# Optimization experiments

Measured on AMD Instinct MI355X. Metric: run time of the kernel, lower is better.

The kernel has to match this reference:

```python
import jax, jax.numpy as jnp
import numpy as np

B, C, W, H, X, Y = 2, 32, 256, 256, 512, 512


def _rbf(x1, x2, ls):
    # x1: [B, N], x2: [B, M] -> [B, N, M]; identical math to norms+matmul pw_dists2 on 1-d coords
    d2 = (x1[:, :, None] - x2[:, None, :]) ** 2
    return jnp.exp(-0.5 * d2 / ls ** 2)


def setup_inputs() -> dict:
    key = jax.random.key(0)
    k0, k1, k2, k3, k4 = jax.random.split(key, 5)
    return {
        "x_in_lon": jax.random.uniform(k0, (B, W), jnp.float32),
        "x_in_lat": jax.random.uniform(k1, (B, H), jnp.float32),
        "wt": jax.random.normal(k2, (B, C, W, H), jnp.float32),
        "x_out_lon": jax.random.uniform(k3, (B, X), jnp.float32),
        "x_out_lat": jax.random.uniform(k4, (B, Y), jnp.float32),
        "init_ls": jnp.full((1,), 0.1, jnp.float32),
    }


def reference(x_in_lon, x_in_lat, wt, x_out_lon, x_out_lat, init_ls):
    # density channel: 1 where data present, 0 where NaN; zero-fill NaNs in data
    dens = jnp.where(jnp.isnan(wt[:, 0:1]), 0.0, 1.0)
    wt_full = jnp.concatenate([dens, jnp.nan_to_num(wt)], axis=1)  # [B, C+1, W, H]
    ls = init_ls[0]
    w_lon = _rbf(x_in_lon, x_out_lon, ls)  # [B, W, X]
    w_lat = _rbf(x_in_lat, x_out_lat, ls)  # [B, H, Y]
    # separable 'OnToOn' contraction: [B,C+1,W,H] x [B,W,X] x [B,H,Y] -> [B,C+1,X,Y]
    ee = jnp.einsum('bcwh,bwx,bhy->bcxy', wt_full, w_lon, w_lat)
    d = jnp.clip(ee[:, 0:1], 1e-6, 1e5)
    return jnp.concatenate([ee[:, 0:1], ee[:, 1:] / d], axis=1)
```

## Files before the change

### kernel.cpp

```cpp
#include <hip/hip_runtime.h>
#include <cstddef>

#define B_ 2
#define C_ 32
#define CP 33
#define W_ 256
#define H_ 256
#define X_ 512
#define Y_ 512

typedef __bf16 bf16x8 __attribute__((ext_vector_type(8)));
typedef __bf16 bf16x4 __attribute__((ext_vector_type(4)));
typedef float  f32x4  __attribute__((ext_vector_type(4)));

#define AS1 __attribute__((address_space(1)))
#define AS3 __attribute__((address_space(3)))

__device__ __forceinline__ void gload16_lds(const void* g, void* l) {
    __builtin_amdgcn_global_load_lds((const AS1 void*)g, (AS3 void*)l, 16, 0, 0);
}


__global__ __launch_bounds__(256) void prep_kernel(
    const float* __restrict__ xin_lon, const float* __restrict__ xin_lat,
    const float* __restrict__ xout_lon, const float* __restrict__ xout_lat,
    const float* __restrict__ init_ls, const float* __restrict__ wt,
    __bf16* __restrict__ wlonF, __bf16* __restrict__ wlatF,
    __bf16* __restrict__ wt33F)
{
    __shared__ __bf16 tile[64 * 130];

    const int t = threadIdx.x;
    const int bid = blockIdx.x;
    float ls = init_ls[0];
    float cc = -0.5f / (ls * ls);

    if (bid < 528) {
        const int p  = bid >> 3, tl = bid & 7;
        const int wq = tl >> 1, hq = tl & 1;
        const int b  = p / CP, ch = p - b * CP;
        const float* src = (ch == 0)
            ? wt + ((size_t)b * C_) * (W_ * H_)
            : wt + ((size_t)b * C_ + (ch - 1)) * (W_ * H_);
        const int rowt = t >> 5, hl = (t & 31) * 4;
#pragma unroll
        for (int i = 0; i < 8; ++i) {
            int rl = i * 8 + rowt;
            const float* sp = src + (size_t)(wq * 64 + rl) * H_ + hq * 128 + hl;
            float4 v = *(const float4*)sp;
            bf16x4 ov;
            if (ch == 0) {
                ov[0] = (__bf16)((v.x != v.x) ? 0.f : 1.f);
                ov[1] = (__bf16)((v.y != v.y) ? 0.f : 1.f);
                ov[2] = (__bf16)((v.z != v.z) ? 0.f : 1.f);
                ov[3] = (__bf16)((v.w != v.w) ? 0.f : 1.f);
            } else {
                ov[0] = (__bf16)((v.x != v.x) ? 0.f : v.x);
                ov[1] = (__bf16)((v.y != v.y) ? 0.f : v.y);
                ov[2] = (__bf16)((v.z != v.z) ? 0.f : v.z);
                ov[3] = (__bf16)((v.w != v.w) ? 0.f : v.w);
            }
            *(bf16x4*)&tile[rl * 130 + hl] = ov;
        }
        __syncthreads();
        const int lane = t & 63, wave = t >> 6;
        __bf16* pb = wt33F + (size_t)p * 65536 + (size_t)(wq >> 1) * 32768;
        const int rfg0 = (wq & 1) * 4, ktg0 = hq * 4;
#pragma unroll
        for (int it = 0; it < 4; ++it) {
            int ci   = it * 4 + wave;
            int kt_l = ci >> 2, rf_l = ci & 3;
            int wl = rf_l * 16 + (lane & 15);
            int hl2 = kt_l * 32 + (lane >> 4) * 8;
            bf16x8 v = *(const bf16x8*)&tile[wl * 130 + hl2];
            *(bf16x8*)&pb[(size_t)((ktg0 + kt_l) * 8 + rfg0 + rf_l) * 512
                          + lane * 8] = v;
        }
    } else {
        int j = (bid - 528) * 256 + t;
        if (j < 32768) {
            int lane = j & 63, nf = (j >> 6) & 3, kt = (j >> 8) & 7;
            int xt = (j >> 11) & 7, b = j >> 14;
            int x  = xt * 64 + nf * 16 + (lane & 15);
            int k0 = kt * 32 + (lane >> 4) * 8;
            float xo = xout_lon[b * X_ + x];
            bf16x8 v;
#pragma unroll
            for (int e = 0; e < 8; ++e) {
                float d = xin_lon[b * W_ + k0 + e] - xo;
                v[e] = (__bf16)__expf(cc * d * d);
            }
            *(bf16x8*)&wlonF[(size_t)j * 8] = v;
        } else {
            int c = j - 32768;
            int lane = c & 63, bfr = (c >> 6) & 3, kt = (c >> 8) & 7;
            int yt = (c >> 11) & 7, b = c >> 14;
            int y  = yt * 64 + bfr * 16 + (lane & 15);
            int h0 = kt * 32 + (lane >> 4) * 8;
            float yo = xout_lat[b * Y_ + y];
            bf16x8 v;
#pragma unroll
            for (int e = 0; e < 8; ++e) {
                float d = xin_lat[b * H_ + h0 + e] - yo;
                v[e] = (__bf16)__expf(cc * d * d);
            }
            *(bf16x8*)&wlatF[(size_t)c * 8] = v;
        }
    }
}

__global__ __launch_bounds__(256, 4) void gemm_u(
    const __bf16* __restrict__ wt33F, const __bf16* __restrict__ wlatF,
    __bf16* __restrict__ U_F)
{
    __shared__ union SM {
        struct { __bf16 A[2][4096]; __bf16 Bt[2][2048]; } t;
        __bf16 th[8704];
    } sm;

    const int t    = threadIdx.x;
    const int lane = t & 63;
    const int wave = t >> 6;
    const int wm   = wave >> 1, wn = wave & 1;
    const int lrow = lane & 15, lkg = lane >> 4;

    const int xcd = blockIdx.x & 7, k = blockIdx.x >> 3;
    const int m   = xcd * 132 + k;
    const int p   = m >> 4, tile = m & 15;
    const int mtile = tile >> 3, ntile = tile & 7;
    const int bb = (p >= CP) ? 1 : 0;
    const __bf16* Abase = wt33F + ((size_t)(p * 2 + mtile)) * 32768;
    const __bf16* Bbase = wlatF + ((size_t)(bb * 8 + ntile)) * 16384;

    auto stage = [&](int buf, int kt) {
#pragma unroll
        for (int j = 0; j < 2; ++j) {
            int rf = j * 4 + wave;
            gload16_lds((const void*)(Abase + (size_t)(kt * 8 + rf) * 512 + lane * 8),
                        (void*)&sm.t.A[buf][rf * 512]);
        }
        gload16_lds((const void*)(Bbase + (size_t)(kt * 4 + wave) * 512 + lane * 8),
                    (void*)&sm.t.Bt[buf][wave * 512]);
    };

    f32x4 acc[4][2] = {};
    stage(0, 0);
#pragma unroll
    for (int kt = 0; kt < 8; ++kt) {
        const int buf = kt & 1;
        if (kt < 7) {
            stage(buf ^ 1, kt + 1);
            asm volatile("s_waitcnt vmcnt(3)" ::: "memory");
        } else {
            asm volatile("s_waitcnt vmcnt(0)" ::: "memory");
        }
        __builtin_amdgcn_s_barrier();
        bf16x8 af[4], bf[2];
#pragma unroll
        for (int mt = 0; mt < 4; ++mt)
            af[mt] = *(const bf16x8*)&sm.t.A[buf][((wm * 4 + mt) * 64 + lane) * 8];
#pragma unroll
        for (int nt = 0; nt < 2; ++nt)
            bf[nt] = *(const bf16x8*)&sm.t.Bt[buf][((wn * 2 + nt) * 64 + lane) * 8];
#pragma unroll
        for (int mt = 0; mt < 4; ++mt)
#pragma unroll
            for (int nt = 0; nt < 2; ++nt)
                acc[mt][nt] = __builtin_amdgcn_mfma_f32_16x16x32_bf16(
                    af[mt], bf[nt], acc[mt][nt], 0, 0, 0);
        __builtin_amdgcn_sched_barrier(0);
        __builtin_amdgcn_s_barrier();
    }

#pragma unroll
    for (int mt = 0; mt < 4; ++mt)
#pragma unroll
        for (int nt = 0; nt < 2; ++nt) {
            int yloc = wn * 32 + nt * 16 + lrow;
            int wloc = wm * 64 + mt * 16 + lkg * 4;
            f32x4 c = acc[mt][nt];
            bf16x4 v4;
            v4[0] = (__bf16)c[0]; v4[1] = (__bf16)c[1];
            v4[2] = (__bf16)c[2]; v4[3] = (__bf16)c[3];
            *(bf16x4*)&sm.th[yloc * 136 + wloc] = v4;
        }
    __syncthreads();
    __bf16* up = U_F + (size_t)p * 131072 + (size_t)ntile * 16384
                 + (size_t)mtile * 4 * 2048;
#pragma unroll
    for (int it = 0; it < 4; ++it) {
        int c2 = it * 256 + t;
        int ktl = c2 >> 8, rq = (c2 >> 6) & 3, ln = c2 & 63;
        int yloc = rq * 16 + (ln & 15);
        int w8   = ktl * 4 + (ln >> 4);
        bf16x8 v = *(const bf16x8*)&sm.th[yloc * 136 + w8 * 8];
        *(bf16x8*)&up[(size_t)(ktl * 4 + rq) * 512 + ln * 8] = v;
    }
}

__global__ __launch_bounds__(256, 2) void stage2_fused(
    const __bf16* __restrict__ wlonF, const __bf16* __restrict__ U_F,
    float* __restrict__ out)
{
    __shared__ __bf16 Ast[2][12288];

    const int t = threadIdx.x, lane = t & 63, wave = t >> 6;
    const int lrow = lane & 15, lkg = lane >> 4;
    const int wm = wave >> 1, wn = wave & 1;

    const int bid  = blockIdx.x;
    const int xcd  = bid & 7, q = bid >> 3;
    const int combo = (q >> 6) * 8 + xcd;
    const int b    = combo >> 3, g = combo & 7;
    const int tile = q & 63;
    const int yt   = tile >> 3, xt = tile & 7;
    const int x0   = xt * 64, y0 = yt * 64;

    const __bf16* lonF  = wlonF + (size_t)(b * 8 + xt) * 16384;
    const __bf16* Ubase = U_F + (size_t)(b * CP) * 131072 + (size_t)yt * 16384;

    auto stage = [&](int slot, int kt) {
#pragma unroll
        for (int i = 0; i < 6; ++i) {
            const int jf = wave * 6 + i;
            const __bf16* src;
            if (jf < 20) {
                const int jj = jf >> 2;
                const int ch = (jj == 0) ? 0 : (g * 4 + jj);
                src = Ubase + (size_t)ch * 131072
                      + (size_t)(kt * 4 + (jf & 3)) * 512 + lane * 8;
            } else {
                src = lonF + (size_t)(kt * 4 + (jf - 20)) * 512 + lane * 8;
            }
            gload16_lds((const void*)src, (void*)&Ast[slot][jf * 512]);
        }
    };

    stage(0, 0);

    f32x4 acc[5][2][2] = {};
#pragma unroll
    for (int kt = 0; kt < 8; ++kt) {
        const int slot = kt & 1;
        if (kt < 7) {
            stage(slot ^ 1, kt + 1);
            asm volatile("s_waitcnt vmcnt(6)" ::: "memory");
        } else {
            asm volatile("s_waitcnt vmcnt(0)" ::: "memory");
        }
        __builtin_amdgcn_s_barrier();
        bf16x8 af[5][2], bfv[2];
#pragma unroll
        for (int j = 0; j < 5; ++j)
#pragma unroll
            for (int mt = 0; mt < 2; ++mt)
                af[j][mt] = *(const bf16x8*)
                    &Ast[slot][((j * 4 + wm * 2 + mt) * 64 + lane) * 8];
#pragma unroll
        for (int nt = 0; nt < 2; ++nt)
            bfv[nt] = *(const bf16x8*)
                &Ast[slot][((20 + wn * 2 + nt) * 64 + lane) * 8];
#pragma unroll
        for (int j = 0; j < 5; ++j)
#pragma unroll
            for (int mt = 0; mt < 2; ++mt)
#pragma unroll
                for (int nt = 0; nt < 2; ++nt)
                    acc[j][mt][nt] = __builtin_amdgcn_mfma_f32_16x16x32_bf16(
                        af[j][mt], bfv[nt], acc[j][mt][nt], 0, 0, 0);
        __builtin_amdgcn_sched_barrier(0);
        __builtin_amdgcn_s_barrier();
    }

    f32x4 rec[2][2];
#pragma unroll
    for (int mt = 0; mt < 2; ++mt)
#pragma unroll
        for (int nt = 0; nt < 2; ++nt) {
            f32x4 c = acc[0][mt][nt], q2;
#pragma unroll
            for (int rr = 0; rr < 4; ++rr)
                q2[rr] = 1.0f / fminf(fmaxf(c[rr], 1e-6f), 1e5f);
            rec[mt][nt] = q2;
        }
    if (g == 0) {
        float* outc = out + (size_t)(b * CP) * (X_ * Y_);
#pragma unroll
        for (int mt = 0; mt < 2; ++mt)
#pragma unroll
            for (int nt = 0; nt < 2; ++nt) {
                int xg = x0 + (wn * 2 + nt) * 16 + lrow;
                int yg = y0 + (wm * 2 + mt) * 16 + lkg * 4;
                *(f32x4*)&outc[(size_t)xg * Y_ + yg] = acc[0][mt][nt];
            }
    }
#pragma unroll
    for (int j = 1; j < 5; ++j) {
        float* outc = out + (size_t)(b * CP + g * 4 + j) * (size_t)(X_ * Y_);
#pragma unroll
        for (int mt = 0; mt < 2; ++mt)
#pragma unroll
            for (int nt = 0; nt < 2; ++nt) {
                int xg = x0 + (wn * 2 + nt) * 16 + lrow;
                int yg = y0 + (wm * 2 + mt) * 16 + lkg * 4;
                f32x4 v = acc[j][mt][nt] * rec[mt][nt];
                *(f32x4*)&outc[(size_t)xg * Y_ + yg] = v;
            }
    }
}

extern "C" void kernel_launch(void* const* d_in, const int* in_sizes, int n_in,
                              void* d_out, int out_size, void* d_ws, size_t ws_size,
                              hipStream_t stream)
{
    const float* xin_lon  = (const float*)d_in[0];
    const float* xin_lat  = (const float*)d_in[1];
    const float* wt       = (const float*)d_in[2];
    const float* xout_lon = (const float*)d_in[3];
    const float* xout_lat = (const float*)d_in[4];
    const float* init_ls  = (const float*)d_in[5];
    float* out = (float*)d_out;

    __bf16* wlonF = (__bf16*)d_ws;
    __bf16* wlatF = wlonF + (size_t)B_ * X_ * W_;
    __bf16* wt33F = wlatF + (size_t)B_ * Y_ * H_;
    __bf16* U_F   = wt33F + (size_t)B_ * CP * W_ * H_;

    prep_kernel<<<784, 256, 0, stream>>>(xin_lon, xin_lat, xout_lon, xout_lat,
                                         init_ls, wt, wlonF, wlatF, wt33F);
    gemm_u<<<1056, 256, 0, stream>>>(wt33F, wlatF, U_F);
    stage2_fused<<<1024, 256, 0, stream>>>(wlonF, U_F, out);
}
```

Baseline: 46.08 us.

## Load MFMA fragments directly from global memory, dropping LDS staging in stage2

```diff
diff --git a/kernel.cpp b/kernel.cpp
--- a/kernel.cpp
+++ b/kernel.cpp
@@ -202,8 +202,6 @@
     const __bf16* __restrict__ wlonF, const __bf16* __restrict__ U_F,
     float* __restrict__ out)
 {
-    __shared__ __bf16 Ast[2][12288];
-
     const int t = threadIdx.x, lane = t & 63, wave = t >> 6;
     const int lrow = lane & 15, lkg = lane >> 4;
     const int wm = wave >> 1, wn = wave & 1;
@@ -216,50 +214,26 @@
     const int yt   = tile >> 3, xt = tile & 7;
     const int x0   = xt * 64, y0 = yt * 64;
 
-    const __bf16* lonF  = wlonF + (size_t)(b * 8 + xt) * 16384;
-    const __bf16* Ubase = U_F + (size_t)(b * CP) * 131072 + (size_t)yt * 16384;
-
-    auto stage = [&](int slot, int kt) {
-#pragma unroll
-        for (int i = 0; i < 6; ++i) {
-            const int jf = wave * 6 + i;
-            const __bf16* src;
-            if (jf < 20) {
-                const int jj = jf >> 2;
-                const int ch = (jj == 0) ? 0 : (g * 4 + jj);
-                src = Ubase + (size_t)ch * 131072
-                      + (size_t)(kt * 4 + (jf & 3)) * 512 + lane * 8;
-            } else {
-                src = lonF + (size_t)(kt * 4 + (jf - 20)) * 512 + lane * 8;
-            }
-            gload16_lds((const void*)src, (void*)&Ast[slot][jf * 512]);
-        }
-    };
-
-    stage(0, 0);
+    const __bf16* lonp = wlonF + (size_t)(b * 8 + xt) * 16384
+                         + (size_t)(wn * 2) * 512 + lane * 8;
+    const __bf16* Au   = U_F + (size_t)(b * CP) * 131072 + (size_t)yt * 16384
+                         + (size_t)(wm * 2) * 512 + lane * 8;
 
     f32x4 acc[5][2][2] = {};
 #pragma unroll
     for (int kt = 0; kt < 8; ++kt) {
-        const int slot = kt & 1;
-        if (kt < 7) {
-            stage(slot ^ 1, kt + 1);
-            asm volatile("s_waitcnt vmcnt(6)" ::: "memory");
-        } else {
-            asm volatile("s_waitcnt vmcnt(0)" ::: "memory");
-        }
-        __builtin_amdgcn_s_barrier();
         bf16x8 af[5][2], bfv[2];
 #pragma unroll
-        for (int j = 0; j < 5; ++j)
+        for (int j = 0; j < 5; ++j) {
+            const int ch = (j == 0) ? 0 : (g * 4 + j);
 #pragma unroll
             for (int mt = 0; mt < 2; ++mt)
-                af[j][mt] = *(const bf16x8*)
-                    &Ast[slot][((j * 4 + wm * 2 + mt) * 64 + lane) * 8];
+                af[j][mt] = *(const bf16x8*)(Au + (size_t)ch * 131072
+                                             + (size_t)(kt * 4 + mt) * 512);
+        }
 #pragma unroll
         for (int nt = 0; nt < 2; ++nt)
-            bfv[nt] = *(const bf16x8*)
-                &Ast[slot][((20 + wn * 2 + nt) * 64 + lane) * 8];
+            bfv[nt] = *(const bf16x8*)(lonp + (size_t)(kt * 4 + nt) * 512);
 #pragma unroll
         for (int j = 0; j < 5; ++j)
 #pragma unroll
@@ -268,8 +242,6 @@
                 for (int nt = 0; nt < 2; ++nt)
                     acc[j][mt][nt] = __builtin_amdgcn_mfma_f32_16x16x32_bf16(
                         af[j][mt], bfv[nt], acc[j][mt][nt], 0, 0, 0);
-        __builtin_amdgcn_sched_barrier(0);
-        __builtin_amdgcn_s_barrier();
     }
 
     f32x4 rec[2][2];
```

Result: slower. 68.77 us (+49.2%).

## Process two channel groups per block, keeping lon tile resident in LDS

Applied to the files above, without the earlier changes.

```diff
diff --git a/kernel.cpp b/kernel.cpp
--- a/kernel.cpp
+++ b/kernel.cpp
@@ -202,110 +202,119 @@
     const __bf16* __restrict__ wlonF, const __bf16* __restrict__ U_F,
     float* __restrict__ out)
 {
-    __shared__ __bf16 Ast[2][12288];
+    __shared__ __bf16 Blon[16384];
+    __shared__ __bf16 Ast[2][10240];
 
     const int t = threadIdx.x, lane = t & 63, wave = t >> 6;
     const int lrow = lane & 15, lkg = lane >> 4;
     const int wm = wave >> 1, wn = wave & 1;
 
     const int bid  = blockIdx.x;
-    const int xcd  = bid & 7, q = bid >> 3;
-    const int combo = (q >> 6) * 8 + xcd;
-    const int b    = combo >> 3, g = combo & 7;
-    const int tile = q & 63;
-    const int yt   = tile >> 3, xt = tile & 7;
+    const int xcd  = bid & 7, r = bid >> 3;
+    const int b    = xcd >> 2, gpair = xcd & 3;
+    const int yt   = r >> 3, xt = r & 7;
     const int x0   = xt * 64, y0 = yt * 64;
+    const int g0   = gpair * 2;
 
     const __bf16* lonF  = wlonF + (size_t)(b * 8 + xt) * 16384;
     const __bf16* Ubase = U_F + (size_t)(b * CP) * 131072 + (size_t)yt * 16384;
 
-    auto stage = [&](int slot, int kt) {
-#pragma unroll
-        for (int i = 0; i < 6; ++i) {
-            const int jf = wave * 6 + i;
-            const __bf16* src;
-            if (jf < 20) {
-                const int jj = jf >> 2;
-                const int ch = (jj == 0) ? 0 : (g * 4 + jj);
-                src = Ubase + (size_t)ch * 131072
-                      + (size_t)(kt * 4 + (jf & 3)) * 512 + lane * 8;
+    {
+#pragma unroll
+        for (int i = 0; i < 8; ++i) {
+            const int f = wave * 8 + i;
+            gload16_lds((const void*)(lonF + (size_t)f * 512 + lane * 8),
+                        (void*)&Blon[f * 512]);
+        }
+    }
+    auto stageA = [&](int slot, int g, int kt) {
+#pragma unroll
+        for (int i = 0; i < 5; ++i) {
+            const int jf = wave * 5 + i;
+            const int jj = jf >> 2;
+            const int ch = (jj == 0) ? 0 : (g * 4 + jj);
+            const __bf16* src = Ubase + (size_t)ch * 131072
+                                + (size_t)(kt * 4 + (jf & 3)) * 512 + lane * 8;
+            gload16_lds((const void*)src, (void*)&Ast[slot][jf * 512]);
+        }
+    };
+
+    stageA(0, g0, 0);
+    stageA(1, g0, 1);
+
+#pragma unroll
+    for (int p = 0; p < 2; ++p) {
+        const int g = g0 + p;
+        f32x4 acc[5][2][2] = {};
+#pragma unroll
+        for (int kt = 0; kt < 8; ++kt) {
+            const int ph = p * 8 + kt;
+            const int slot = ph & 1;
+            if (ph < 15) {
+                stageA(slot ^ 1, g0 + ((ph + 1) >> 3), (ph + 1) & 7);
+                asm volatile("s_waitcnt vmcnt(5)" ::: "memory");
             } else {
-                src = lonF + (size_t)(kt * 4 + (jf - 20)) * 512 + lane * 8;
-            }
-            gload16_lds((const void*)src, (void*)&Ast[slot][jf * 512]);
-        }
-    };
-
-    stage(0, 0);
-
-    f32x4 acc[5][2][2] = {};
-#pragma unroll
-    for (int kt = 0; kt < 8; ++kt) {
-        const int slot = kt & 1;
-        if (kt < 7) {
-            stage(slot ^ 1, kt + 1);
-            asm volatile("s_waitcnt vmcnt(6)" ::: "memory");
-        } else {
-            asm volatile("s_waitcnt vmcnt(0)" ::: "memory");
-        }
-        __builtin_amdgcn_s_barrier();
-        bf16x8 af[5][2], bfv[2];
-#pragma unroll
-        for (int j = 0; j < 5; ++j)
+                asm volatile("s_waitcnt vmcnt(0)" ::: "memory");
+            }
+            __builtin_amdgcn_s_barrier();
+            bf16x8 af[5][2], bfv[2];
+#pragma unroll
+            for (int j = 0; j < 5; ++j)
+#pragma unroll
+                for (int mt = 0; mt < 2; ++mt)
+                    af[j][mt] = *(const bf16x8*)
+                        &Ast[slot][((j * 4 + wm * 2 + mt) * 64 + lane) * 8];
+#pragma unroll
+            for (int nt = 0; nt < 2; ++nt)
+                bfv[nt] = *(const bf16x8*)
+                    &Blon[((kt * 4 + wn * 2 + nt) * 64 + lane) * 8];
+#pragma unroll
+            for (int j = 0; j < 5; ++j)
+#pragma unroll
+                for (int mt = 0; mt < 2; ++mt)
+#pragma unroll
+                    for (int nt = 0; nt < 2; ++nt)
+                        acc[j][mt][nt] = __builtin_amdgcn_mfma_f32_16x16x32_bf16(
+                            af[j][mt], bfv[nt], acc[j][mt][nt], 0, 0, 0);
+            __builtin_amdgcn_sched_barrier(0);
+            __builtin_amdgcn_s_barrier();
+        }
+
+        f32x4 rec[2][2];
+#pragma unroll
+        for (int mt = 0; mt < 2; ++mt)
+#pragma unroll
+            for (int nt = 0; nt < 2; ++nt) {
+                f32x4 c = acc[0][mt][nt], q2;
+#pragma unroll
+                for (int rr = 0; rr < 4; ++rr)
+                    q2[rr] = 1.0f / fminf(fmaxf(c[rr], 1e-6f), 1e5f);
+                rec[mt][nt] = q2;
+            }
+        if (g == 0) {
+            float* outc = out + (size_t)(b * CP) * (X_ * Y_);
 #pragma unroll
             for (int mt = 0; mt < 2; ++mt)
-                af[j][mt] = *(const bf16x8*)
-                    &Ast[slot][((j * 4 + wm * 2 + mt) * 64 + lane) * 8];
-#pragma unroll
-        for (int nt = 0; nt < 2; ++nt)
-            bfv[nt] = *(const bf16x8*)
-                &Ast[slot][((20 + wn * 2 + nt) * 64 + lane) * 8];
-#pragma unroll
-        for (int j = 0; j < 5; ++j)
+#pragma unroll
+                for (int nt = 0; nt < 2; ++nt) {
+                    int xg = x0 + (wn * 2 + nt) * 16 + lrow;
+                    int yg = y0 + (wm * 2 + mt) * 16 + lkg * 4;
+                    *(f32x4*)&outc[(size_t)xg * Y_ + yg] = acc[0][mt][nt];
+                }
+        }
+#pragma unroll
+        for (int j = 1; j < 5; ++j) {
+            float* outc = out + (size_t)(b * CP + g * 4 + j) * (size_t)(X_ * Y_);
 #pragma unroll
             for (int mt = 0; mt < 2; ++mt)
 #pragma unroll
-                for (int nt = 0; nt < 2; ++nt)
-                    acc[j][mt][nt] = __builtin_amdgcn_mfma_f32_16x16x32_bf16(
-                        af[j][mt], bfv[nt], acc[j][mt][nt], 0, 0, 0);
-        __builtin_amdgcn_sched_barrier(0);
-        __builtin_amdgcn_s_barrier();
-    }
-
-    f32x4 rec[2][2];
-#pragma unroll
-    for (int mt = 0; mt < 2; ++mt)
-#pragma unroll
-        for (int nt = 0; nt < 2; ++nt) {
-            f32x4 c = acc[0][mt][nt], q2;
-#pragma unroll
-            for (int rr = 0; rr < 4; ++rr)
-                q2[rr] = 1.0f / fminf(fmaxf(c[rr], 1e-6f), 1e5f);
-            rec[mt][nt] = q2;
-        }
-    if (g == 0) {
-        float* outc = out + (size_t)(b * CP) * (X_ * Y_);
-#pragma unroll
-        for (int mt = 0; mt < 2; ++mt)
-#pragma unroll
-            for (int nt = 0; nt < 2; ++nt) {
-                int xg = x0 + (wn * 2 + nt) * 16 + lrow;
-                int yg = y0 + (wm * 2 + mt) * 16 + lkg * 4;
-                *(f32x4*)&outc[(size_t)xg * Y_ + yg] = acc[0][mt][nt];
-            }
-    }
-#pragma unroll
-    for (int j = 1; j < 5; ++j) {
-        float* outc = out + (size_t)(b * CP + g * 4 + j) * (size_t)(X_ * Y_);
-#pragma unroll
-        for (int mt = 0; mt < 2; ++mt)
-#pragma unroll
-            for (int nt = 0; nt < 2; ++nt) {
-                int xg = x0 + (wn * 2 + nt) * 16 + lrow;
-                int yg = y0 + (wm * 2 + mt) * 16 + lkg * 4;
-                f32x4 v = acc[j][mt][nt] * rec[mt][nt];
-                *(f32x4*)&outc[(size_t)xg * Y_ + yg] = v;
-            }
+                for (int nt = 0; nt < 2; ++nt) {
+                    int xg = x0 + (wn * 2 + nt) * 16 + lrow;
+                    int yg = y0 + (wm * 2 + mt) * 16 + lkg * 4;
+                    f32x4 v = acc[j][mt][nt] * rec[mt][nt];
+                    *(f32x4*)&outc[(size_t)xg * Y_ + yg] = v;
+                }
+        }
     }
 }
 
@@ -329,5 +338,5 @@
     prep_kernel<<<784, 256, 0, stream>>>(xin_lon, xin_lat, xout_lon, xout_lat,
                                          init_ls, wt, wlonF, wlatF, wt33F);
     gemm_u<<<1056, 256, 0, stream>>>(wt33F, wlatF, U_F);
-    stage2_fused<<<1024, 256, 0, stream>>>(wlonF, U_F, out);
-}
+    stage2_fused<<<512, 256, 0, stream>>>(wlonF, U_F, out);
+}
```

Result: slower. 47.08 us (+2.2%).

## Fuse NaN-fill and bf16 conversion of input field into first GEMM

Applied to the files above, without the earlier changes.

```diff
diff --git a/kernel.cpp b/kernel.cpp
--- a/kernel.cpp
+++ b/kernel.cpp
@@ -21,33 +21,98 @@
 }
 
 
-__global__ __launch_bounds__(256) void prep_kernel(
+__global__ __launch_bounds__(256) void prep_tables(
     const float* __restrict__ xin_lon, const float* __restrict__ xin_lat,
     const float* __restrict__ xout_lon, const float* __restrict__ xout_lat,
-    const float* __restrict__ init_ls, const float* __restrict__ wt,
-    __bf16* __restrict__ wlonF, __bf16* __restrict__ wlatF,
-    __bf16* __restrict__ wt33F)
+    const float* __restrict__ init_ls,
+    __bf16* __restrict__ wlonF, __bf16* __restrict__ wlatF)
 {
-    __shared__ __bf16 tile[64 * 130];
-
-    const int t = threadIdx.x;
-    const int bid = blockIdx.x;
+    int j = blockIdx.x * 256 + threadIdx.x;
     float ls = init_ls[0];
     float cc = -0.5f / (ls * ls);
-
-    if (bid < 528) {
-        const int p  = bid >> 3, tl = bid & 7;
-        const int wq = tl >> 1, hq = tl & 1;
-        const int b  = p / CP, ch = p - b * CP;
-        const float* src = (ch == 0)
-            ? wt + ((size_t)b * C_) * (W_ * H_)
-            : wt + ((size_t)b * C_ + (ch - 1)) * (W_ * H_);
-        const int rowt = t >> 5, hl = (t & 31) * 4;
-#pragma unroll
-        for (int i = 0; i < 8; ++i) {
-            int rl = i * 8 + rowt;
-            const float* sp = src + (size_t)(wq * 64 + rl) * H_ + hq * 128 + hl;
-            float4 v = *(const float4*)sp;
+    if (j < 32768) {
+        int lane = j & 63, nf = (j >> 6) & 3, kt = (j >> 8) & 7;
+        int xt = (j >> 11) & 7, b = j >> 14;
+        int x  = xt * 64 + nf * 16 + (lane & 15);
+        int k0 = kt * 32 + (lane >> 4) * 8;
+        float xo = xout_lon[b * X_ + x];
+        bf16x8 v;
+#pragma unroll
+        for (int e = 0; e < 8; ++e) {
+            float d = xin_lon[b * W_ + k0 + e] - xo;
+            v[e] = (__bf16)__expf(cc * d * d);
+        }
+        *(bf16x8*)&wlonF[(size_t)j * 8] = v;
+    } else {
+        int c = j - 32768;
+        int lane = c & 63, bfr = (c >> 6) & 3, kt = (c >> 8) & 7;
+        int yt = (c >> 11) & 7, b = c >> 14;
+        int y  = yt * 64 + bfr * 16 + (lane & 15);
+        int h0 = kt * 32 + (lane >> 4) * 8;
+        float yo = xout_lat[b * Y_ + y];
+        bf16x8 v;
+#pragma unroll
+        for (int e = 0; e < 8; ++e) {
+            float d = xin_lat[b * H_ + h0 + e] - yo;
+            v[e] = (__bf16)__expf(cc * d * d);
+        }
+        *(bf16x8*)&wlatF[(size_t)c * 8] = v;
+    }
+}
+
+__global__ __launch_bounds__(256, 2) void gemm_u(
+    const float* __restrict__ wt, const __bf16* __restrict__ wlatF,
+    __bf16* __restrict__ U_F)
+{
+    __shared__ union SM {
+        struct { __bf16 At[128 * 136]; __bf16 Bl[8192]; } t;
+        __bf16 th[8704];
+    } sm;
+
+    const int t    = threadIdx.x;
+    const int lane = t & 63;
+    const int wave = t >> 6;
+    const int wm   = wave >> 1, wn = wave & 1;
+    const int lrow = lane & 15, lkg = lane >> 4;
+
+    const int xcd = blockIdx.x & 7, k = blockIdx.x >> 3;
+    const int m   = xcd * 132 + k;
+    const int p   = m >> 4, tile = m & 15;
+    const int mtile = tile >> 3, ntile = tile & 7;
+    const int bb = (p >= CP) ? 1 : 0;
+    const int ch = p - bb * CP;
+
+    const __bf16* Bbase = wlatF + ((size_t)(bb * 8 + ntile)) * 16384;
+    auto stageB = [&](int half) {
+#pragma unroll
+        for (int i = 0; i < 4; ++i) {
+            int jf = wave * 4 + i;
+            gload16_lds((const void*)(Bbase + (size_t)(half * 16 + jf) * 512
+                                      + lane * 8),
+                        (void*)&sm.t.Bl[jf * 512]);
+        }
+    };
+    stageB(0);
+
+    const float* src = (ch == 0)
+        ? wt + ((size_t)bb * C_) * (W_ * H_)
+        : wt + ((size_t)bb * C_ + (ch - 1)) * (W_ * H_);
+    src += (size_t)mtile * 128 * H_;
+
+    const int rquad = t >> 5;
+    const int c4    = (t & 31) * 4;
+
+    f32x4 acc[4][2] = {};
+#pragma unroll
+    for (int half = 0; half < 2; ++half) {
+        if (half) {
+            __syncthreads();
+            stageB(1);
+        }
+#pragma unroll 4
+        for (int i = 0; i < 16; ++i) {
+            int r = i * 8 + rquad;
+            float4 v = *(const float4*)(src + (size_t)r * H_ + half * 128 + c4);
             bf16x4 ov;
             if (ch == 0) {
                 ov[0] = (__bf16)((v.x != v.x) ? 0.f : 1.f);
@@ -60,117 +125,30 @@
                 ov[2] = (__bf16)((v.z != v.z) ? 0.f : v.z);
                 ov[3] = (__bf16)((v.w != v.w) ? 0.f : v.w);
             }
-            *(bf16x4*)&tile[rl * 130 + hl] = ov;
-        }
+            *(bf16x4*)&sm.t.At[r * 136 + c4] = ov;
+        }
+        asm volatile("s_waitcnt vmcnt(0)" ::: "memory");
         __syncthreads();
-        const int lane = t & 63, wave = t >> 6;
-        __bf16* pb = wt33F + (size_t)p * 65536 + (size_t)(wq >> 1) * 32768;
-        const int rfg0 = (wq & 1) * 4, ktg0 = hq * 4;
-#pragma unroll
-        for (int it = 0; it < 4; ++it) {
-            int ci   = it * 4 + wave;
-            int kt_l = ci >> 2, rf_l = ci & 3;
-            int wl = rf_l * 16 + (lane & 15);
-            int hl2 = kt_l * 32 + (lane >> 4) * 8;
-            bf16x8 v = *(const bf16x8*)&tile[wl * 130 + hl2];
-            *(bf16x8*)&pb[(size_t)((ktg0 + kt_l) * 8 + rfg0 + rf_l) * 512
-                          + lane * 8] = v;
-        }
-    } else {
-        int j = (bid - 528) * 256 + t;
-        if (j < 32768) {
-            int lane = j & 63, nf = (j >> 6) & 3, kt = (j >> 8) & 7;
-            int xt = (j >> 11) & 7, b = j >> 14;
-            int x  = xt * 64 + nf * 16 + (lane & 15);
-            int k0 = kt * 32 + (lane >> 4) * 8;
-            float xo = xout_lon[b * X_ + x];
-            bf16x8 v;
-#pragma unroll
-            for (int e = 0; e < 8; ++e) {
-                float d = xin_lon[b * W_ + k0 + e] - xo;
-                v[e] = (__bf16)__expf(cc * d * d);
-            }
-            *(bf16x8*)&wlonF[(size_t)j * 8] = v;
-        } else {
-            int c = j - 32768;
-            int lane = c & 63, bfr = (c >> 6) & 3, kt = (c >> 8) & 7;
-            int yt = (c >> 11) & 7, b = c >> 14;
-            int y  = yt * 64 + bfr * 16 + (lane & 15);
-            int h0 = kt * 32 + (lane >> 4) * 8;
-            float yo = xout_lat[b * Y_ + y];
-            bf16x8 v;
-#pragma unroll
-            for (int e = 0; e < 8; ++e) {
-                float d = xin_lat[b * H_ + h0 + e] - yo;
-                v[e] = (__bf16)__expf(cc * d * d);
-            }
-            *(bf16x8*)&wlatF[(size_t)c * 8] = v;
-        }
-    }
-}
-
-__global__ __launch_bounds__(256, 4) void gemm_u(
-    const __bf16* __restrict__ wt33F, const __bf16* __restrict__ wlatF,
-    __bf16* __restrict__ U_F)
-{
-    __shared__ union SM {
-        struct { __bf16 A[2][4096]; __bf16 Bt[2][2048]; } t;
-        __bf16 th[8704];
-    } sm;
-
-    const int t    = threadIdx.x;
-    const int lane = t & 63;
-    const int wave = t >> 6;
-    const int wm   = wave >> 1, wn = wave & 1;
-    const int lrow = lane & 15, lkg = lane >> 4;
-
-    const int xcd = blockIdx.x & 7, k = blockIdx.x >> 3;
-    const int m   = xcd * 132 + k;
-    const int p   = m >> 4, tile = m & 15;
-    const int mtile = tile >> 3, ntile = tile & 7;
-    const int bb = (p >= CP) ? 1 : 0;
-    const __bf16* Abase = wt33F + ((size_t)(p * 2 + mtile)) * 32768;
-    const __bf16* Bbase = wlatF + ((size_t)(bb * 8 + ntile)) * 16384;
-
-    auto stage = [&](int buf, int kt) {
-#pragma unroll
-        for (int j = 0; j < 2; ++j) {
-            int rf = j * 4 + wave;
-            gload16_lds((const void*)(Abase + (size_t)(kt * 8 + rf) * 512 + lane * 8),
-                        (void*)&sm.t.A[buf][rf * 512]);
-        }
-        gload16_lds((const void*)(Bbase + (size_t)(kt * 4 + wave) * 512 + lane * 8),
-                    (void*)&sm.t.Bt[buf][wave * 512]);
-    };
-
-    f32x4 acc[4][2] = {};
-    stage(0, 0);
-#pragma unroll
-    for (int kt = 0; kt < 8; ++kt) {
-        const int buf = kt & 1;
-        if (kt < 7) {
-            stage(buf ^ 1, kt + 1);
-            asm volatile("s_waitcnt vmcnt(3)" ::: "memory");
-        } else {
-            asm volatile("s_waitcnt vmcnt(0)" ::: "memory");
-        }
-        __builtin_amdgcn_s_barrier();
-        bf16x8 af[4], bf[2];
-#pragma unroll
-        for (int mt = 0; mt < 4; ++mt)
-            af[mt] = *(const bf16x8*)&sm.t.A[buf][((wm * 4 + mt) * 64 + lane) * 8];
-#pragma unroll
-        for (int nt = 0; nt < 2; ++nt)
-            bf[nt] = *(const bf16x8*)&sm.t.Bt[buf][((wn * 2 + nt) * 64 + lane) * 8];
-#pragma unroll
-        for (int mt = 0; mt < 4; ++mt)
+#pragma unroll
+        for (int kt = 0; kt < 4; ++kt) {
+            bf16x8 af[4], bf[2];
+#pragma unroll
+            for (int mt = 0; mt < 4; ++mt)
+                af[mt] = *(const bf16x8*)
+                    &sm.t.At[(wm * 64 + mt * 16 + lrow) * 136 + kt * 32 + lkg * 8];
 #pragma unroll
             for (int nt = 0; nt < 2; ++nt)
-                acc[mt][nt] = __builtin_amdgcn_mfma_f32_16x16x32_bf16(
-                    af[mt], bf[nt], acc[mt][nt], 0, 0, 0);
-        __builtin_amdgcn_sched_barrier(0);
-        __builtin_amdgcn_s_barrier();
-    }
+                bf[nt] = *(const bf16x8*)
+                    &sm.t.Bl[((kt * 4 + wn * 2 + nt) * 64 + lane) * 8];
+#pragma unroll
+            for (int mt = 0; mt < 4; ++mt)
+#pragma unroll
+                for (int nt = 0; nt < 2; ++nt)
+                    acc[mt][nt] = __builtin_amdgcn_mfma_f32_16x16x32_bf16(
+                        af[mt], bf[nt], acc[mt][nt], 0, 0, 0);
+        }
+    }
+    __syncthreads();
 
 #pragma unroll
     for (int mt = 0; mt < 4; ++mt)
@@ -260,6 +238,8 @@
         for (int nt = 0; nt < 2; ++nt)
             bfv[nt] = *(const bf16x8*)
                 &Ast[slot][((20 + wn * 2 + nt) * 64 + lane) * 8];
+        asm volatile("s_waitcnt lgkmcnt(0)" ::: "memory");
+        __builtin_amdgcn_sched_barrier(0);
 #pragma unroll
         for (int j = 0; j < 5; ++j)
 #pragma unroll
@@ -323,11 +303,10 @@
 
     __bf16* wlonF = (__bf16*)d_ws;
     __bf16* wlatF = wlonF + (size_t)B_ * X_ * W_;
-    __bf16* wt33F = wlatF + (size_t)B_ * Y_ * H_;
-    __bf16* U_F   = wt33F + (size_t)B_ * CP * W_ * H_;
-
-    prep_kernel<<<784, 256, 0, stream>>>(xin_lon, xin_lat, xout_lon, xout_lat,
-                                         init_ls, wt, wlonF, wlatF, wt33F);
-    gemm_u<<<1056, 256, 0, stream>>>(wt33F, wlatF, U_F);
+    __bf16* U_F   = wlatF + (size_t)B_ * Y_ * H_;
+
+    prep_tables<<<256, 256, 0, stream>>>(xin_lon, xin_lat, xout_lon, xout_lat,
+                                         init_ls, wlonF, wlatF);
+    gemm_u<<<1056, 256, 0, stream>>>(wt, wlatF, U_F);
     stage2_fused<<<1024, 256, 0, stream>>>(wlonF, U_F, out);
 }
```

Result: slower. 60.13 us (+30.5%).
